# Performance work log

Measured on AMD Instinct MI355X. Metric: run time of the kernel, lower is better.

Reference implementation:

```python
import jax, jax.numpy as jnp
import numpy as np

N, IN, H0, H1 = 8192, 128, 512, 256
ITER = 10
EPS = 1e-5


def _bn(h, g, b):
    # BatchNorm1d in training mode: biased batch stats
    mu = h.mean(axis=0)
    var = h.var(axis=0)
    return g * (h - mu) * jax.lax.rsqrt(var + EPS) + b


def setup_inputs() -> dict:
    key = jax.random.key(0)
    ks = jax.random.split(key, 8)
    x = jax.random.normal(ks[0], (N, IN), dtype=jnp.float32)
    W = jax.random.uniform(ks[1], (N, N), dtype=jnp.float32)  # torch.rand
    W1 = jax.random.normal(ks[2], (H0, IN), dtype=jnp.float32) * (1.0 / np.sqrt(IN))
    b1 = jnp.zeros((H0,), jnp.float32)
    g1 = jnp.ones((H0,), jnp.float32)
    be1 = jnp.zeros((H0,), jnp.float32)
    W2 = jax.random.normal(ks[3], (H1, H0), dtype=jnp.float32) * (1.0 / np.sqrt(H0))
    b2 = jnp.zeros((H1,), jnp.float32)
    g2 = jnp.ones((H1,), jnp.float32)
    be2 = jnp.zeros((H1,), jnp.float32)
    fcw = jax.random.normal(ks[4], (1, H1), dtype=jnp.float32) * (1.0 / np.sqrt(H1))
    fcb = jnp.zeros((1,), jnp.float32)
    return {"x": x, "W": W, "W1": W1, "b1": b1, "g1": g1, "be1": be1,
            "W2": W2, "b2": b2, "g2": g2, "be2": be2, "fcw": fcw, "fcb": fcb}


def reference(x, W, W1, b1, g1, be1, W2, b2, g2, be2, fcw, fcb):
    h = jax.nn.leaky_relu(_bn(x @ W1.T + b1, g1, be1), 0.01)        # [N, H0]
    feats = jax.nn.leaky_relu(_bn(h @ W2.T + b2, g2, be2), 0.01)    # [N, H1]
    logits = feats @ fcw.T + fcb                                    # [N, 1]
    fn = jnp.linalg.norm(feats, axis=1, keepdims=True)              # [N, 1]
    pairwise_sim = (feats @ feats.T) / (fn @ fn.T)                  # [N, N]
    W_sym = (W + W.T) * 0.5
    PP = pairwise_sim * W_sym                                       # [N, N]
    unary = logits
    def body(i, lg):
        coef = 1.0 - 2.0 * jax.nn.sigmoid(lg)                       # (1-p) - p, [N,1]
        # E_i = sum_j (1-2 p_j) * PP[i, j]  -> matvec
        return unary + PP @ coef
    logits = jax.lax.fori_loop(0, ITER, body, logits)
    return logits
```

## Files before the change

kernel.cpp:

```cpp
#include <hip/hip_runtime.h>
#include <hip/hip_bf16.h>

#define NROWS 8192
#define NITER 10

typedef __attribute__((ext_vector_type(8))) short bf16x8;
typedef __attribute__((ext_vector_type(8))) unsigned short u16x8;
typedef __attribute__((ext_vector_type(16))) float f32x16;

__device__ __forceinline__ float bf2f(unsigned short u) {
  union { float f; unsigned int i; } c; c.i = ((unsigned int)u) << 16; return c.f;
}
__device__ __forceinline__ unsigned short f2bf(float f) {
  unsigned int x = __float_as_uint(f);
  unsigned int r = (x + 0x7FFFu + ((x >> 16) & 1u)) >> 16;
  return (unsigned short)r;
}

#define TRIS(b) ((b) * (257 - (b)) / 2)
__device__ __forceinline__ void tril_decode(int L, int& bi, int& bj) {
  int b = (int)((257.0f - sqrtf((float)(66049 - 8 * L))) * 0.5f);
  if (b > 127) b = 127;
  if (b < 0) b = 0;
  while (b < 127 && TRIS(b + 1) <= L) ++b;
  while (b > 0 && TRIS(b) > L) --b;
  bi = b;
  bj = b + (L - TRIS(b));
}

__global__ __launch_bounds__(256) void cast3(const float* __restrict__ x,
                                             const float* __restrict__ W1,
                                             const float* __restrict__ W2,
                                             unsigned short* __restrict__ xb,
                                             unsigned short* __restrict__ w1b,
                                             unsigned short* __restrict__ w2b) {
  int idx = blockIdx.x * 256 + threadIdx.x;
  const float* src; unsigned short* dst; int l;
  if (idx < 131072) { src = x; dst = xb; l = idx; }
  else if (idx < 139264) { src = W1; dst = w1b; l = idx - 131072; }
  else if (idx < 155648) { src = W2; dst = w2b; l = idx - 139264; }
  else return;
  const float4* p = (const float4*)src + (size_t)l * 2;
  float4 a = p[0], b = p[1];
  u16x8 o;
  o[0] = f2bf(a.x); o[1] = f2bf(a.y); o[2] = f2bf(a.z); o[3] = f2bf(a.w);
  o[4] = f2bf(b.x); o[5] = f2bf(b.y); o[6] = f2bf(b.z); o[7] = f2bf(b.w);
  *(u16x8*)(dst + (size_t)l * 8) = o;
}

__global__ __launch_bounds__(256) void gemm_bt_mfma_stats(
    const unsigned short* __restrict__ A, const unsigned short* __restrict__ B,
    unsigned short* __restrict__ Cb, float* __restrict__ pS, float* __restrict__ pQ,
    int NN, int K) {
  __shared__ __align__(16) unsigned short Asw[4096];
  __shared__ __align__(16) unsigned short Bsw[4096];
  __shared__ float Sarr[4][64], Qarr[4][64];
  const int i0 = blockIdx.x * 64, j0 = blockIdx.y * 64;
  const int t = threadIdx.x;
  const int lane = t & 63;
  const int wv = t >> 6;
  const int wi = wv >> 1, wj = wv & 1;
  const int khalf = lane >> 5;

  f32x16 acc;
#pragma unroll
  for (int r = 0; r < 16; ++r) acc[r] = 0.f;

  const int lrow = t >> 2;
  const int lgp = (t & 3) * 2;
  const int arow = wi * 32 + (lane & 31);
  const int brow = wj * 32 + (lane & 31);
  const int nc = K >> 6;
#pragma unroll 1
  for (int c = 0; c < nc; ++c) {
    const unsigned short* sa = A + (size_t)(i0 + lrow) * K + c * 64 + lgp * 8;
    const unsigned short* sb = B + (size_t)(j0 + lrow) * K + c * 64 + lgp * 8;
    u16x8 va0 = *(const u16x8*)(sa);
    u16x8 va1 = *(const u16x8*)(sa + 8);
    u16x8 vb0 = *(const u16x8*)(sb);
    u16x8 vb1 = *(const u16x8*)(sb + 8);
    __syncthreads();
    int s0 = (lgp ^ (lrow & 7)) * 8;
    int s1 = ((lgp + 1) ^ (lrow & 7)) * 8;
    *(u16x8*)&Asw[lrow * 64 + s0] = va0;
    *(u16x8*)&Asw[lrow * 64 + s1] = va1;
    *(u16x8*)&Bsw[lrow * 64 + s0] = vb0;
    *(u16x8*)&Bsw[lrow * 64 + s1] = vb1;
    __syncthreads();
#pragma unroll
    for (int s = 0; s < 4; ++s) {
      int slot = s * 2 + khalf;
      bf16x8 a = *(const bf16x8*)&Asw[arow * 64 + ((slot ^ (arow & 7)) * 8)];
      bf16x8 b = *(const bf16x8*)&Bsw[brow * 64 + ((slot ^ (brow & 7)) * 8)];
      acc = __builtin_amdgcn_mfma_f32_32x32x16_bf16(a, b, acc, 0, 0, 0);
    }
  }
  float s = 0.f, q = 0.f;
#pragma unroll
  for (int r = 0; r < 16; ++r) {
    int rowl = (r & 3) + 8 * (r >> 2) + 4 * khalf;
    int coll = lane & 31;
    float v = acc[r];
    s += v; q += v * v;
    Cb[(size_t)(i0 + wi * 32 + rowl) * NN + j0 + wj * 32 + coll] = f2bf(v);
  }
  Sarr[wv][lane] = s;
  Qarr[wv][lane] = q;
  __syncthreads();
  if (t < 64) {
    int wjc = t >> 5, coll = t & 31;
    float st = (Sarr[wjc][coll] + Sarr[wjc][coll + 32]) +
               (Sarr[wjc + 2][coll] + Sarr[wjc + 2][coll + 32]);
    float qt = (Qarr[wjc][coll] + Qarr[wjc][coll + 32]) +
               (Qarr[wjc + 2][coll] + Qarr[wjc + 2][coll + 32]);
    pS[(size_t)blockIdx.x * NN + j0 + t] = st;
    pQ[(size_t)blockIdx.x * NN + j0 + t] = qt;
  }
}

__global__ void bn_finalize(const float* __restrict__ pS, const float* __restrict__ pQ,
                            const float* __restrict__ g, const float* __restrict__ be,
                            float2* __restrict__ ab, int C) {
  int c = blockIdx.x * 256 + threadIdx.x;
  if (c >= C) return;
  float s = 0.f, q = 0.f;
  for (int r = 0; r < 128; ++r) { s += pS[(size_t)r * C + c]; q += pQ[(size_t)r * C + c]; }
  const float invM = 1.f / 8192.f;
  float mu = s * invM;
  float var = q * invM - mu * mu;
  float rstd = rsqrtf(var + 1e-5f);
  float a = g[c] * rstd;
  ab[c] = make_float2(a, be[c] - mu * a);
}

__global__ __launch_bounds__(256) void bn_apply(const unsigned short* __restrict__ hraw,
                                                const float2* __restrict__ ab,
                                                unsigned short* __restrict__ hb,
                                                int Cmask) {
  size_t idx = (size_t)blockIdx.x * 256 + threadIdx.x;
  u16x8 v = *(const u16x8*)(hraw + idx * 8);
  int cb = (int)((idx * 8) & (size_t)Cmask);
  u16x8 o;
#pragma unroll
  for (int k = 0; k < 8; ++k) {
    float2 a = ab[cb + k];
    float r = a.x * bf2f(v[k]) + a.y;
    r = r >= 0.f ? r : 0.01f * r;
    o[k] = f2bf(r);
  }
  *(u16x8*)(hb + idx * 8) = o;
}

__global__ __launch_bounds__(256) void bn_rowfn(const unsigned short* __restrict__ fraw,
                                                const float2* __restrict__ ab,
                                                const float* __restrict__ fcw,
                                                const float* __restrict__ fcb,
                                                unsigned short* __restrict__ fnorm,
                                                float* __restrict__ unary,
                                                float* __restrict__ coef0) {
  const int lane = threadIdx.x & 63;
  const int row = blockIdx.x * 4 + (threadIdx.x >> 6);
  ushort4 v4 = *(const ushort4*)(fraw + (size_t)row * 256 + lane * 4);
  float4 w = *(const float4*)(fcw + lane * 4);
  int c = lane * 4;
  float2 a0 = ab[c], a1 = ab[c + 1], a2 = ab[c + 2], a3 = ab[c + 3];
  float f0 = a0.x * bf2f(v4.x) + a0.y; f0 = f0 >= 0.f ? f0 : 0.01f * f0;
  float f1 = a1.x * bf2f(v4.y) + a1.y; f1 = f1 >= 0.f ? f1 : 0.01f * f1;
  float f2 = a2.x * bf2f(v4.z) + a2.y; f2 = f2 >= 0.f ? f2 : 0.01f * f2;
  float f3 = a3.x * bf2f(v4.w) + a3.y; f3 = f3 >= 0.f ? f3 : 0.01f * f3;
  float ssq = f0 * f0 + f1 * f1 + f2 * f2 + f3 * f3;
  float dot = f0 * w.x + f1 * w.y + f2 * w.z + f3 * w.w;
#pragma unroll
  for (int o = 32; o; o >>= 1) { ssq += __shfl_xor(ssq, o); dot += __shfl_xor(dot, o); }
  float rfn = rsqrtf(ssq);
  *(ushort4*)(fnorm + (size_t)row * 256 + lane * 4) =
      make_ushort4(f2bf(f0 * rfn), f2bf(f1 * rfn), f2bf(f2 * rfn), f2bf(f3 * rfn));
  if (lane == 0) {
    float lg = dot + fcb[0];
    unary[row] = lg;
    coef0[row] = 1.f - 2.f / (1.f + __expf(-lg));
  }
}

__global__ __launch_bounds__(256) void ppbuild_sym(const unsigned short* __restrict__ fnorm,
                                                   const float* __restrict__ W,
                                                   unsigned short* __restrict__ PP) {
  int bi, bj;
  tril_decode(blockIdx.x, bi, bj);
  const int i0 = bi * 64, j0 = bj * 64;

  __shared__ __align__(16) unsigned char shm[18944];
  unsigned short* Asw = (unsigned short*)shm;
  unsigned short* Bsw = (unsigned short*)shm + 4736;
  float (*Wt)[68] = (float(*)[68])shm;
  unsigned short* OutD = (unsigned short*)shm;

  const int t = threadIdx.x;
  const int lane = t & 63;
  const int wv = t >> 6;
  const int wi = wv >> 1, wj = wv & 1;
  const int khalf = lane >> 5;

  f32x16 acc;
#pragma unroll
  for (int r = 0; r < 16; ++r) acc[r] = 0.f;

  const int lrow = t >> 2;
  const int lgp = (t & 3) * 2;
  const int arow = wi * 32 + (lane & 31);
  const int brow = wj * 32 + (lane & 31);
#pragma unroll 1
  for (int c = 0; c < 4; ++c) {
    const unsigned short* sa = fnorm + (size_t)(i0 + lrow) * 256 + c * 64 + lgp * 8;
    const unsigned short* sb = fnorm + (size_t)(j0 + lrow) * 256 + c * 64 + lgp * 8;
    u16x8 va0 = *(const u16x8*)(sa);
    u16x8 va1 = *(const u16x8*)(sa + 8);
    u16x8 vb0 = *(const u16x8*)(sb);
    u16x8 vb1 = *(const u16x8*)(sb + 8);
    __syncthreads();
    int s0 = (lgp ^ (lrow & 7)) * 8;
    int s1 = ((lgp + 1) ^ (lrow & 7)) * 8;
    *(u16x8*)&Asw[lrow * 64 + s0] = va0;
    *(u16x8*)&Asw[lrow * 64 + s1] = va1;
    *(u16x8*)&Bsw[lrow * 64 + s0] = vb0;
    *(u16x8*)&Bsw[lrow * 64 + s1] = vb1;
    __syncthreads();
#pragma unroll
    for (int s = 0; s < 4; ++s) {
      int slot = s * 2 + khalf;
      bf16x8 a = *(const bf16x8*)&Asw[arow * 64 + ((slot ^ (arow & 7)) * 8)];
      bf16x8 b = *(const bf16x8*)&Bsw[brow * 64 + ((slot ^ (brow & 7)) * 8)];
      acc = __builtin_amdgcn_mfma_f32_32x32x16_bf16(a, b, acc, 0, 0, 0);
    }
  }

  __syncthreads();
  {
    const int j = t >> 2, cb = (t & 3) * 16;
    const float* src = W + (size_t)(j0 + j) * NROWS + i0 + cb;
#pragma unroll
    for (int q = 0; q < 4; ++q) {
      float4 v = *(const float4*)(src + q * 4);
      Wt[j][cb + q * 4 + 0] = v.x; Wt[j][cb + q * 4 + 1] = v.y;
      Wt[j][cb + q * 4 + 2] = v.z; Wt[j][cb + q * 4 + 3] = v.w;
    }
  }
  __syncthreads();
  unsigned short pb[16];
#pragma unroll
  for (int r = 0; r < 16; ++r) {
    int rowl = (r & 3) + 8 * (r >> 2) + 4 * khalf;
    int coll = lane & 31;
    int il = wi * 32 + rowl, jl = wj * 32 + coll;
    float wd = W[(size_t)(i0 + il) * NROWS + (j0 + jl)];
    float ws = 0.5f * (wd + Wt[jl][il]);
    pb[r] = f2bf(acc[r] * ws);
  }
  __syncthreads();
#pragma unroll
  for (int r = 0; r < 16; ++r) {
    int rowl = (r & 3) + 8 * (r >> 2) + 4 * khalf;
    int coll = lane & 31;
    OutD[(wi * 32 + rowl) * 74 + wj * 32 + coll] = pb[r];
  }
  __syncthreads();
  const int row = t >> 3;
  const int seg = t & 7;
#pragma unroll
  for (int q = 0; q < 2; ++q) {
    int rr = row + q * 32;
    const unsigned int* pd = (const unsigned int*)(OutD + rr * 74 + seg * 8);
    union { u16x8 v; unsigned int u[4]; } dd;
#pragma unroll
    for (int k = 0; k < 4; ++k) dd.u[k] = pd[k];
    *(u16x8*)(PP + (size_t)(i0 + rr) * NROWS + j0 + seg * 8) = dd.v;
  }
}

__global__ __launch_bounds__(256) void ppmv_sym(const unsigned short* __restrict__ PP,
                                                const float* __restrict__ coef_in,
                                                float* __restrict__ pE) {
  int bi, bj;
  tril_decode(blockIdx.x, bi, bj);
  const int i0 = bi * 64, j0 = bj * 64;
  const int t = threadIdx.x;

  __shared__ unsigned short tile[64][68];
  __shared__ float cj[64], ci[64], Tw[4][64], Dred[64];
  if (t < 64) cj[t] = coef_in[j0 + t];
  else if (t < 128) ci[t - 64] = coef_in[i0 + (t - 64)];
  {
    int r = t >> 2, c0 = (t & 3) * 16;
    const unsigned short* src = PP + (size_t)(i0 + r) * NROWS + j0 + c0;
    u16x8 v0 = *(const u16x8*)(src);
    u16x8 v1 = *(const u16x8*)(src + 8);
    *(u16x8*)&tile[r][c0] = v0;
    *(u16x8*)&tile[r][c0 + 8] = v1;
  }
  __syncthreads();
  {
    int r = t >> 2, c0 = (t & 3) * 16;
    float a = 0.f;
#pragma unroll
    for (int k = 0; k < 16; ++k) a += bf2f(tile[r][c0 + k]) * cj[c0 + k];
    a += __shfl_xor(a, 1);
    a += __shfl_xor(a, 2);
    if ((t & 3) == 0) Dred[r] = a;
  }
  {
    int c = t & 63, w = t >> 6;
    float a = 0.f;
#pragma unroll
    for (int k = 0; k < 16; ++k) a += bf2f(tile[w * 16 + k][c]) * ci[w * 16 + k];
    Tw[w][c] = a;
  }
  __syncthreads();
  if (t < 64) {
    pE[(size_t)bj * NROWS + i0 + t] = Dred[t];
    if (bi != bj) {
      float s = (Tw[0][t] + Tw[1][t]) + (Tw[2][t] + Tw[3][t]);
      pE[(size_t)bi * NROWS + j0 + t] = s;
    }
  }
}

__global__ __launch_bounds__(128) void ppmv_reduce(const float* __restrict__ pE,
                                                   const float* __restrict__ unary,
                                                   float* __restrict__ coef_out,
                                                   float* __restrict__ lg_out) {
  int row = blockIdx.x * 128 + threadIdx.x;
  float acc = 0.f;
#pragma unroll 8
  for (int s = 0; s < 128; ++s) acc += pE[(size_t)s * NROWS + row];
  float lg = unary[row] + acc;
  coef_out[row] = 1.f - 2.f / (1.f + __expf(-lg));
  if (lg_out) lg_out[row] = lg;
}

extern "C" void kernel_launch(void* const* d_in, const int* in_sizes, int n_in,
                              void* d_out, int out_size, void* d_ws, size_t ws_size,
                              hipStream_t stream) {
  const float* x   = (const float*)d_in[0];
  const float* W   = (const float*)d_in[1];
  const float* W1  = (const float*)d_in[2];
  const float* g1  = (const float*)d_in[4];
  const float* be1 = (const float*)d_in[5];
  const float* W2  = (const float*)d_in[6];
  const float* g2  = (const float*)d_in[8];
  const float* be2 = (const float*)d_in[9];
  const float* fcw = (const float*)d_in[10];
  const float* fcb = (const float*)d_in[11];
  float* out = (float*)d_out;

  char* ws = (char*)d_ws;
  unsigned short* hraw = (unsigned short*)(ws + 0);
  float* pE    = (float*)(ws + 0);
  unsigned short* fraw = (unsigned short*)(ws + 8388608);
  float* pS1   = (float*)(ws + 12582912);
  float* pQ1   = (float*)(ws + 12845056);
  float* pS2   = (float*)(ws + 13107200);
  float* pQ2   = (float*)(ws + 13238272);
  float2* ab1  = (float2*)(ws + 13369344);
  float2* ab2  = (float2*)(ws + 13373440);
  unsigned short* fnorm = (unsigned short*)(ws + 13375488);
  float* unary = (float*)(ws + 17569792);
  float* coefA = (float*)(ws + 17602560);
  float* coefB = (float*)(ws + 17635328);
  unsigned short* hb  = (unsigned short*)(ws + 17668096);
  unsigned short* xb  = (unsigned short*)(ws + 26056704);
  unsigned short* w1b = (unsigned short*)(ws + 28153856);
  unsigned short* w2b = (unsigned short*)(ws + 28284928);
  unsigned short* PP  = (unsigned short*)(ws + 28547072);
  if (ws_size < (size_t)162764800) return;

  cast3<<<608, 256, 0, stream>>>(x, W1, W2, xb, w1b, w2b);
  gemm_bt_mfma_stats<<<dim3(128, 8), 256, 0, stream>>>(xb, w1b, hraw, pS1, pQ1, 512, 128);
  bn_finalize<<<2, 256, 0, stream>>>(pS1, pQ1, g1, be1, ab1, 512);
  bn_apply<<<2048, 256, 0, stream>>>(hraw, ab1, hb, 511);
  gemm_bt_mfma_stats<<<dim3(128, 4), 256, 0, stream>>>(hb, w2b, fraw, pS2, pQ2, 256, 512);
  bn_finalize<<<1, 256, 0, stream>>>(pS2, pQ2, g2, be2, ab2, 256);
  bn_rowfn<<<2048, 256, 0, stream>>>(fraw, ab2, fcw, fcb, fnorm, unary, coefA);
  ppbuild_sym<<<8256, 256, 0, stream>>>(fnorm, W, PP);
  float* cur = coefA; float* nxt = coefB;
  for (int it = 0; it < NITER; ++it) {
    ppmv_sym<<<8256, 256, 0, stream>>>(PP, cur, pE);
    ppmv_reduce<<<64, 128, 0, stream>>>(pE, unary, nxt, it == NITER - 1 ? out : nullptr);
    float* tmp = cur; cur = nxt; nxt = tmp;
  }
}
```

Before: 339.5 us.

## Enlarge symmetric matvec tiles to 128x128 and vectorize shared-memory reads

The symmetric PP matvec now uses 128x128 lower-triangle tiles instead of 64x64. This cuts the block count from 8256 to 2080 and halves the number of partial-sum rows the reduce kernel must read. The inner loops now use vectorized LDS loads (u16x8, float4, ushort4), and the reduce kernel moves to 256-thread blocks. In exchange, each block uses more LDS (about 38KB), which may lower occupancy. It also leaves fewer blocks to hide memory latency.

```diff
diff --git a/kernel.cpp b/kernel.cpp
--- a/kernel.cpp
+++ b/kernel.cpp
@@ -26,6 +26,17 @@
   while (b > 0 && TRIS(b) > L) --b;
   bi = b;
   bj = b + (L - TRIS(b));
+}
+
+#define TRIS64(b) ((b) * (129 - (b)) / 2)
+__device__ __forceinline__ void tril64_decode(int L, int& bi, int& bj) {
+  int b = (int)((129.0f - sqrtf((float)(16641 - 8 * L))) * 0.5f);
+  if (b > 63) b = 63;
+  if (b < 0) b = 0;
+  while (b < 63 && TRIS64(b + 1) <= L) ++b;
+  while (b > 0 && TRIS64(b) > L) --b;
+  bi = b;
+  bj = b + (L - TRIS64(b));
 }
 
 __global__ __launch_bounds__(256) void cast3(const float* __restrict__ x,
@@ -281,57 +292,72 @@
                                                 const float* __restrict__ coef_in,
                                                 float* __restrict__ pE) {
   int bi, bj;
-  tril_decode(blockIdx.x, bi, bj);
-  const int i0 = bi * 64, j0 = bj * 64;
+  tril64_decode(blockIdx.x, bi, bj);
+  const int i0 = bi * 128, j0 = bj * 128;
   const int t = threadIdx.x;
 
-  __shared__ unsigned short tile[64][68];
-  __shared__ float cj[64], ci[64], Tw[4][64], Dred[64];
-  if (t < 64) cj[t] = coef_in[j0 + t];
-  else if (t < 128) ci[t - 64] = coef_in[i0 + (t - 64)];
+  __shared__ __align__(16) unsigned short tile[128][132];
+  __shared__ float cj[128], ci[128];
+  __shared__ float Tw[8][128];
+  __shared__ float Dred[128];
+
+  if (t < 128) cj[t] = coef_in[j0 + t];
+  else ci[t - 128] = coef_in[i0 + (t - 128)];
   {
-    int r = t >> 2, c0 = (t & 3) * 16;
-    const unsigned short* src = PP + (size_t)(i0 + r) * NROWS + j0 + c0;
-    u16x8 v0 = *(const u16x8*)(src);
-    u16x8 v1 = *(const u16x8*)(src + 8);
-    *(u16x8*)&tile[r][c0] = v0;
-    *(u16x8*)&tile[r][c0 + 8] = v1;
+    const int r = t >> 1, h = (t & 1) * 64;
+    const unsigned short* src = PP + (size_t)(i0 + r) * NROWS + j0 + h;
+#pragma unroll
+    for (int q = 0; q < 8; ++q)
+      *(u16x8*)&tile[r][h + q * 8] = *(const u16x8*)(src + q * 8);
   }
   __syncthreads();
   {
-    int r = t >> 2, c0 = (t & 3) * 16;
+    const int r = t >> 1, h = (t & 1) * 64;
     float a = 0.f;
 #pragma unroll
-    for (int k = 0; k < 16; ++k) a += bf2f(tile[r][c0 + k]) * cj[c0 + k];
+    for (int q = 0; q < 8; ++q) {
+      u16x8 v = *(const u16x8*)&tile[r][h + q * 8];
+      float4 c0 = *(const float4*)&cj[h + q * 8];
+      float4 c1 = *(const float4*)&cj[h + q * 8 + 4];
+      a += bf2f(v[0]) * c0.x + bf2f(v[1]) * c0.y + bf2f(v[2]) * c0.z + bf2f(v[3]) * c0.w;
+      a += bf2f(v[4]) * c1.x + bf2f(v[5]) * c1.y + bf2f(v[6]) * c1.z + bf2f(v[7]) * c1.w;
+    }
     a += __shfl_xor(a, 1);
-    a += __shfl_xor(a, 2);
-    if ((t & 3) == 0) Dred[r] = a;
+    if ((t & 1) == 0) Dred[r] = a;
   }
   {
-    int c = t & 63, w = t >> 6;
-    float a = 0.f;
-#pragma unroll
-    for (int k = 0; k < 16; ++k) a += bf2f(tile[w * 16 + k][c]) * ci[w * 16 + k];
-    Tw[w][c] = a;
-  }
-  __syncthreads();
-  if (t < 64) {
+    const int c4 = (t & 31) * 4, rg = t >> 5;
+    float a0 = 0.f, a1 = 0.f, a2 = 0.f, a3 = 0.f;
+#pragma unroll
+    for (int k = 0; k < 16; ++k) {
+      int row = rg * 16 + k;
+      ushort4 v = *(const ushort4*)&tile[row][c4];
+      float s = ci[row];
+      a0 += bf2f(v.x) * s; a1 += bf2f(v.y) * s;
+      a2 += bf2f(v.z) * s; a3 += bf2f(v.w) * s;
+    }
+    Tw[rg][c4] = a0; Tw[rg][c4 + 1] = a1;
+    Tw[rg][c4 + 2] = a2; Tw[rg][c4 + 3] = a3;
+  }
+  __syncthreads();
+  if (t < 128) {
     pE[(size_t)bj * NROWS + i0 + t] = Dred[t];
     if (bi != bj) {
-      float s = (Tw[0][t] + Tw[1][t]) + (Tw[2][t] + Tw[3][t]);
+      float s = ((Tw[0][t] + Tw[1][t]) + (Tw[2][t] + Tw[3][t])) +
+                ((Tw[4][t] + Tw[5][t]) + (Tw[6][t] + Tw[7][t]));
       pE[(size_t)bi * NROWS + j0 + t] = s;
     }
   }
 }
 
-__global__ __launch_bounds__(128) void ppmv_reduce(const float* __restrict__ pE,
+__global__ __launch_bounds__(256) void ppmv_reduce(const float* __restrict__ pE,
                                                    const float* __restrict__ unary,
                                                    float* __restrict__ coef_out,
                                                    float* __restrict__ lg_out) {
-  int row = blockIdx.x * 128 + threadIdx.x;
+  int row = blockIdx.x * 256 + threadIdx.x;
   float acc = 0.f;
 #pragma unroll 8
-  for (int s = 0; s < 128; ++s) acc += pE[(size_t)s * NROWS + row];
+  for (int s = 0; s < 64; ++s) acc += pE[(size_t)s * NROWS + row];
   float lg = unary[row] + acc;
   coef_out[row] = 1.f - 2.f / (1.f + __expf(-lg));
   if (lg_out) lg_out[row] = lg;
@@ -383,8 +409,8 @@
   ppbuild_sym<<<8256, 256, 0, stream>>>(fnorm, W, PP);
   float* cur = coefA; float* nxt = coefB;
   for (int it = 0; it < NITER; ++it) {
-    ppmv_sym<<<8256, 256, 0, stream>>>(PP, cur, pE);
-    ppmv_reduce<<<64, 128, 0, stream>>>(pE, unary, nxt, it == NITER - 1 ? out : nullptr);
+    ppmv_sym<<<2080, 256, 0, stream>>>(PP, cur, pE);
+    ppmv_reduce<<<32, 256, 0, stream>>>(pE, unary, nxt, it == NITER - 1 ? out : nullptr);
     float* tmp = cur; cur = nxt; nxt = tmp;
   }
 }
```

Result: faster. 326.0 us (-4.0%).
